# Optimization experiments

Hardware: AMD Instinct MI355X
Metric: run time of the kernel (lower is better)

The kernel has to match this reference:

```python
import jax, jax.numpy as jnp
import numpy as np

N_NODES = 50000
N_EDGES = 800000
IN_DIM = 128
HID = 64
ZDIM = 64
N_GRAPHS = 64


def gcn_conv(x, W, b, src, dst, n):
    # PyG GCNConv: add self-loops, symmetric deg^-1/2 normalization,
    # linear transform then gather-scatter aggregation.
    h = x @ W  # [N, out]
    loops = jnp.arange(n, dtype=src.dtype)
    s = jnp.concatenate([src, loops])
    d = jnp.concatenate([dst, loops])
    deg = jnp.zeros((n,), h.dtype).at[d].add(1.0)  # includes self-loops -> >=1
    dinv = jax.lax.rsqrt(deg)
    norm = dinv[s] * dinv[d]  # [E+N]
    msg = h[s] * norm[:, None]  # gather [E+N, out]
    out = jnp.zeros_like(h).at[d].add(msg)  # scatter-add
    return out + b


def mean_pool(h, batch, num_graphs):
    sums = jax.ops.segment_sum(h, batch, num_segments=num_graphs)
    cnt = jax.ops.segment_sum(jnp.ones((h.shape[0],), h.dtype), batch,
                              num_segments=num_graphs)
    return sums / jnp.maximum(cnt, 1.0)[:, None]


def setup_inputs() -> dict:
    key = jax.random.key(0)
    ks = jax.random.split(key, 9)
    x = jax.random.normal(ks[0], (N_NODES, IN_DIM), jnp.float32)
    edge_index = jax.random.randint(ks[1], (2, N_EDGES), 0, N_NODES, jnp.int64 if jax.config.jax_enable_x64 else jnp.int32)
    batch = jnp.sort(jax.random.randint(ks[2], (N_NODES,), 0, N_GRAPHS))
    s1 = 1.0 / np.sqrt(IN_DIM)
    s2 = 1.0 / np.sqrt(HID)
    W1 = jax.random.uniform(ks[3], (IN_DIM, HID), jnp.float32, -s1, s1)
    b1 = jnp.zeros((HID,), jnp.float32)
    Wmu = jax.random.uniform(ks[4], (HID, ZDIM), jnp.float32, -s2, s2)
    bmu = jnp.zeros((ZDIM,), jnp.float32)
    Wsig = jax.random.uniform(ks[5], (HID, ZDIM), jnp.float32, -s2, s2)
    bsig = jnp.zeros((ZDIM,), jnp.float32)
    return {"x": x, "edge_index": edge_index, "batch": batch,
            "num_graphs": N_GRAPHS, "W1": W1, "b1": b1,
            "Wmu": Wmu, "bmu": bmu, "Wsig": Wsig, "bsig": bsig}


def reference(x, edge_index, batch, num_graphs, W1, b1, Wmu, bmu, Wsig, bsig):
    src, dst = edge_index[0], edge_index[1]
    n = x.shape[0]
    h = jax.nn.elu(gcn_conv(x, W1, b1, src, dst, n))
    z_mu = mean_pool(jax.nn.elu(gcn_conv(h, Wmu, bmu, src, dst, n)), batch, num_graphs)
    z_sigma = mean_pool(jax.nn.elu(gcn_conv(h, Wsig, bsig, src, dst, n)), batch, num_graphs)
    return (z_mu, z_sigma)
```

## Files before the change

### kernel.cpp

```cpp
#include <hip/hip_runtime.h>
#include <hip/hip_fp16.h>


#define IN_DIM 128
#define HID 64
#define ZDIM 64
#define N_GRAPHS 64
#define SCAN_B 1024

typedef _Float16 half8 __attribute__((ext_vector_type(8)));
typedef float f32x4 __attribute__((ext_vector_type(4)));

__device__ __forceinline__ float elu1(float x) {
    return x > 0.f ? x : expm1f(x);
}

#define ACC8(RV, MV) do { \
    const __half2* _hp = (const __half2*)&(RV); \
    float2 _f0 = __half22float2(_hp[0]); \
    float2 _f1 = __half22float2(_hp[1]); \
    float2 _f2 = __half22float2(_hp[2]); \
    float2 _f3 = __half22float2(_hp[3]); \
    acc[0] = fmaf((MV), _f0.x, acc[0]); \
    acc[1] = fmaf((MV), _f0.y, acc[1]); \
    acc[2] = fmaf((MV), _f1.x, acc[2]); \
    acc[3] = fmaf((MV), _f1.y, acc[3]); \
    acc[4] = fmaf((MV), _f2.x, acc[4]); \
    acc[5] = fmaf((MV), _f2.y, acc[5]); \
    acc[6] = fmaf((MV), _f3.x, acc[6]); \
    acc[7] = fmaf((MV), _f3.y, acc[7]); \
  } while (0)

__global__ __launch_bounds__(256) void k_count_wfrag(const int* __restrict__ dst,
                                                     int* __restrict__ kc,
                                                     int* __restrict__ rank, int E,
                                                     const float* __restrict__ W1,
                                                     const float* __restrict__ Wmu,
                                                     const float* __restrict__ Wsig,
                                                     __half* __restrict__ F1,
                                                     __half* __restrict__ Fmu,
                                                     __half* __restrict__ Fsig,
                                                     int cntBlocks) {
    if ((int)blockIdx.x < cntBlocks) {
        int e = (blockIdx.x * 256 + threadIdx.x) * 2;
        if (e + 1 < E) {
            int2 d2 = *(const int2*)&dst[e];
            int r0 = atomicAdd(&kc[d2.x], 1);
            int r1 = atomicAdd(&kc[d2.y], 1);
            *(int2*)&rank[e] = make_int2(r0, r1);
        } else if (e < E) {
            rank[e] = atomicAdd(&kc[dst[e]], 1);
        }
        return;
    }
    int e = (blockIdx.x - cntBlocks) * 256 + threadIdx.x;
    if (e < 8192) {
        int j = e & 7, l = (e >> 3) & 63, ct = (e >> 9) & 3, ks = e >> 11;
        F1[e] = __float2half(W1[(ks * 32 + ((l >> 4) & 3) * 8 + j) * 64 + ct * 16 + (l & 15)]);
    }
    if (e < 4096) {
        int j = e & 7, l = (e >> 3) & 63, ct = (e >> 9) & 3, ks = e >> 11;
        int widx = (ks * 32 + ((l >> 4) & 3) * 8 + j) * 64 + ct * 16 + (l & 15);
        Fmu[e] = __float2half(Wmu[widx]);
        Fsig[e] = __float2half(Wsig[widx]);
    }
}

__global__ __launch_bounds__(SCAN_B) void k_scan1(const int* __restrict__ kc,
                                                  int* __restrict__ bsum, int n) {
    __shared__ int wpart[16];
    int tid = threadIdx.x, lane = tid & 63, w = tid >> 6;
    int i = blockIdx.x * SCAN_B + tid;
    int v = (i < n) ? kc[i] : 0;
#pragma unroll
    for (int d = 1; d < 64; d <<= 1) v += __shfl_xor(v, d, 64);
    if (lane == 0) wpart[w] = v;
    __syncthreads();
    if (tid < 16) {
        int t = wpart[tid];
#pragma unroll
        for (int d = 1; d < 16; d <<= 1) t += __shfl_xor(t, d, 64);
        if (tid == 0) bsum[blockIdx.x] = t;
    }
}

__global__ __launch_bounds__(SCAN_B) void k_scan3(const int* __restrict__ kc,
                                                  const int* __restrict__ bsum,
                                                  int* __restrict__ offs,
                                                  float* __restrict__ dinv,
                                                  int n, int nb) {
    __shared__ int wsum[16];
    __shared__ int sbase;
    int tid = threadIdx.x, lane = tid & 63, w = tid >> 6;
    if (tid < 64) {
        int v = (tid < nb) ? bsum[tid] : 0;
        int s = v;
#pragma unroll
        for (int d = 1; d < 64; d <<= 1) {
            int u = __shfl_up(s, d, 64);
            if (tid >= d) s += u;
        }
        if (tid == blockIdx.x) sbase = s - v;
    }
    int i = blockIdx.x * SCAN_B + tid;
    int v = (i < n) ? kc[i] : 0;
    int s = v;
#pragma unroll
    for (int d = 1; d < 64; d <<= 1) {
        int u = __shfl_up(s, d, 64);
        if (lane >= d) s += u;
    }
    if (lane == 63) wsum[w] = s;
    __syncthreads();
    if (tid < 16) {
        int t = wsum[tid];
#pragma unroll
        for (int d = 1; d < 16; d <<= 1) {
            int u = __shfl_up(t, d, 64);
            if (tid >= d) t += u;
        }
        wsum[tid] = t;
    }
    __syncthreads();
    int base = sbase + ((w == 0) ? 0 : wsum[w - 1]);
    if (i < n) {
        offs[i + 1] = base + s;
        dinv[i] = 1.0f / sqrtf(1.0f + (float)v);
        if (i == 0) offs[0] = 0;
    }
}

__global__ __launch_bounds__(256) void k_fill_mm1(const int* __restrict__ src,
                                                  const int* __restrict__ dst,
                                                  const int* __restrict__ rank,
                                                  const int* __restrict__ offs,
                                                  int* __restrict__ csr, int E,
                                                  const float* __restrict__ x,
                                                  const __half* __restrict__ F1,
                                                  const float* __restrict__ dinv,
                                                  __half* __restrict__ tsA,
                                                  __half* __restrict__ tsB, int n,
                                                  int fillBlocks) {
    if ((int)blockIdx.x < fillBlocks) {
        int e = (blockIdx.x * 256 + threadIdx.x) * 2;
        if (e + 1 < E) {
            int2 s2 = *(const int2*)&src[e];
            int2 d2 = *(const int2*)&dst[e];
            int2 r2 = *(const int2*)&rank[e];
            csr[offs[d2.x] + r2.x] = s2.x;
            csr[offs[d2.y] + r2.y] = s2.y;
        } else if (e < E) {
            csr[offs[dst[e]] + rank[e]] = src[e];
        }
        return;
    }
    int bid = blockIdx.x - fillBlocks;
    int l = threadIdx.x & 63;
    int wave = threadIdx.x >> 6;
    int m0 = bid * 64 + wave * 16;
    int row_a = m0 + (l & 15);
    if (row_a >= n) row_a = n - 1;
    int kg = l >> 4;

    f32x4 acc0 = {0.f, 0.f, 0.f, 0.f};
    f32x4 acc1 = acc0, acc2 = acc0, acc3 = acc0;

    const float* xr = x + (size_t)row_a * IN_DIM + kg * 8;
#pragma unroll
    for (int ks = 0; ks < 4; ++ks) {
        float4 xa = *(const float4*)(xr + ks * 32);
        float4 xb = *(const float4*)(xr + ks * 32 + 4);
        half8 a;
        a[0] = (_Float16)xa.x; a[1] = (_Float16)xa.y;
        a[2] = (_Float16)xa.z; a[3] = (_Float16)xa.w;
        a[4] = (_Float16)xb.x; a[5] = (_Float16)xb.y;
        a[6] = (_Float16)xb.z; a[7] = (_Float16)xb.w;
        const __half* fb = F1 + ((size_t)(ks * 4) * 64 + l) * 8;
        half8 b0 = *(const half8*)(fb);
        half8 b1 = *(const half8*)(fb + 512);
        half8 b2 = *(const half8*)(fb + 1024);
        half8 b3 = *(const half8*)(fb + 1536);
        acc0 = __builtin_amdgcn_mfma_f32_16x16x32_f16(a, b0, acc0, 0, 0, 0);
        acc1 = __builtin_amdgcn_mfma_f32_16x16x32_f16(a, b1, acc1, 0, 0, 0);
        acc2 = __builtin_amdgcn_mfma_f32_16x16x32_f16(a, b2, acc2, 0, 0, 0);
        acc3 = __builtin_amdgcn_mfma_f32_16x16x32_f16(a, b3, acc3, 0, 0, 0);
    }
    int col = l & 15;
#pragma unroll
    for (int r = 0; r < 4; ++r) {
        int row = m0 + kg * 4 + r;
        if (row < n) {
            float di = dinv[row];
            __half* pA = &tsA[(size_t)row * 32 + col];
            pA[0]  = __float2half(acc0[r] * di);
            pA[16] = __float2half(acc1[r] * di);
            __half* pB = &tsB[(size_t)row * 32 + col];
            pB[0]  = __float2half(acc2[r] * di);
            pB[16] = __float2half(acc3[r] * di);
        }
    }
}

__global__ __launch_bounds__(256) void k_gather_hh(const int* __restrict__ off,
                                                   const int* __restrict__ csr,
                                                   const float* __restrict__ dinv,
                                                   const __half* __restrict__ tsA,
                                                   const __half* __restrict__ tsB,
                                                   const float* __restrict__ b1,
                                                   __half* __restrict__ hhA,
                                                   __half* __restrict__ hhB, int n) {
    int bid = blockIdx.x;
    int half = (bid >> 2) & 1;
    int jb = (bid >> 3) * 4 + (bid & 3);
    int wv = threadIdx.x >> 6;
    int node0 = jb * 8 + wv * 2;
    if (node0 >= n) return;
    const __half* T = half ? tsB : tsA;
    __half* H = half ? hhB : hhA;
    int lane = threadIdx.x & 63;
    int nsel = lane >> 5;
    int node = node0 + nsel;
    bool valid = node < n;
    int nodec = valid ? node : n - 1;
    int l32 = lane & 31, g = l32 >> 2, sub = l32 & 3;
    int s0 = off[nodec], s1 = off[nodec + 1];
    float acc[8];
#pragma unroll
    for (int j = 0; j < 8; ++j) acc[j] = 0.f;

    if (s1 > s0) {
        int last = s1 - 1;
        int p0 = s0 + g, p1 = p0 + 8, p2 = p0 + 16, p3 = p0 + 24;
        int i0 = csr[p0 < s1 ? p0 : last];
        int i1 = csr[p1 < s1 ? p1 : last];
        int i2 = csr[p2 < s1 ? p2 : last];
        int i3 = csr[p3 < s1 ? p3 : last];
        float4 r0 = *(const float4*)&T[(size_t)i0 * 32 + sub * 8];
        float4 r1 = *(const float4*)&T[(size_t)i1 * 32 + sub * 8];
        float4 r2 = *(const float4*)&T[(size_t)i2 * 32 + sub * 8];
        float4 r3 = *(const float4*)&T[(size_t)i3 * 32 + sub * 8];
        float m0 = (p0 < s1) ? 1.f : 0.f;
        float m1 = (p1 < s1) ? 1.f : 0.f;
        float m2 = (p2 < s1) ? 1.f : 0.f;
        float m3 = (p3 < s1) ? 1.f : 0.f;
        ACC8(r0, m0);
        ACC8(r1, m1);
        ACC8(r2, m2);
        ACC8(r3, m3);
        for (int k = s0 + 32 + g; k < s1; k += 8) {
            int iv = csr[k];
            float4 rv = *(const float4*)&T[(size_t)iv * 32 + sub * 8];
            ACC8(rv, 1.f);
        }
    }

#pragma unroll
    for (int j = 0; j < 8; ++j) {
        acc[j] += __shfl_xor(acc[j], 4, 64);
        acc[j] += __shfl_xor(acc[j], 8, 64);
        acc[j] += __shfl_xor(acc[j], 16, 64);
    }

    if (g == 0 && valid) {
        int e0 = sub * 8;
        float4 sr = *(const float4*)&T[(size_t)nodec * 32 + e0];
        const __half2* sh = (const __half2*)&sr;
        float di = dinv[nodec];
        const float* bh = b1 + half * 32 + e0;
        float4 ba = *(const float4*)bh;
        float4 bb = *(const float4*)(bh + 4);
        float2 f0 = __half22float2(sh[0]);
        float2 f1 = __half22float2(sh[1]);
        float2 f2 = __half22float2(sh[2]);
        float2 f3 = __half22float2(sh[3]);
        float e0v = elu1((acc[0] + f0.x) * di + ba.x) * di;
        float e1v = elu1((acc[1] + f0.y) * di + ba.y) * di;
        float e2v = elu1((acc[2] + f1.x) * di + ba.z) * di;
        float e3v = elu1((acc[3] + f1.y) * di + ba.w) * di;
        float e4v = elu1((acc[4] + f2.x) * di + bb.x) * di;
        float e5v = elu1((acc[5] + f2.y) * di + bb.y) * di;
        float e6v = elu1((acc[6] + f3.x) * di + bb.z) * di;
        float e7v = elu1((acc[7] + f3.y) * di + bb.w) * di;
        float4 outv;
        __half2* op = (__half2*)&outv;
        op[0] = __floats2half2_rn(e0v, e1v);
        op[1] = __floats2half2_rn(e2v, e3v);
        op[2] = __floats2half2_rn(e4v, e5v);
        op[3] = __floats2half2_rn(e6v, e7v);
        *(float4*)&H[(size_t)node * 32 + e0] = outv;
    }
}

__global__ __launch_bounds__(256) void k_gather_g(const int* __restrict__ off,
                                                  const int* __restrict__ csr,
                                                  const float* __restrict__ dinv,
                                                  const __half* __restrict__ hhA,
                                                  const __half* __restrict__ hhB,
                                                  __half* __restrict__ gh2, int n) {
    int bid = blockIdx.x;
    int half = (bid >> 2) & 1;
    int jb = (bid >> 3) * 4 + (bid & 3);
    int wv = threadIdx.x >> 6;
    int node0 = jb * 8 + wv * 2;
    if (node0 >= n) return;
    const __half* T = half ? hhB : hhA;
    int lane = threadIdx.x & 63;
    int nsel = lane >> 5;
    int node = node0 + nsel;
    bool valid = node < n;
    int nodec = valid ? node : n - 1;
    int l32 = lane & 31, g = l32 >> 2, sub = l32 & 3;
    int s0 = off[nodec], s1 = off[nodec + 1];
    float acc[8];
#pragma unroll
    for (int j = 0; j < 8; ++j) acc[j] = 0.f;

    if (s1 > s0) {
        int last = s1 - 1;
        int p0 = s0 + g, p1 = p0 + 8, p2 = p0 + 16, p3 = p0 + 24;
        int i0 = csr[p0 < s1 ? p0 : last];
        int i1 = csr[p1 < s1 ? p1 : last];
        int i2 = csr[p2 < s1 ? p2 : last];
        int i3 = csr[p3 < s1 ? p3 : last];
        float4 r0 = *(const float4*)&T[(size_t)i0 * 32 + sub * 8];
        float4 r1 = *(const float4*)&T[(size_t)i1 * 32 + sub * 8];
        float4 r2 = *(const float4*)&T[(size_t)i2 * 32 + sub * 8];
        float4 r3 = *(const float4*)&T[(size_t)i3 * 32 + sub * 8];
        float m0 = (p0 < s1) ? 1.f : 0.f;
        float m1 = (p1 < s1) ? 1.f : 0.f;
        float m2 = (p2 < s1) ? 1.f : 0.f;
        float m3 = (p3 < s1) ? 1.f : 0.f;
        ACC8(r0, m0);
        ACC8(r1, m1);
        ACC8(r2, m2);
        ACC8(r3, m3);
        for (int k = s0 + 32 + g; k < s1; k += 8) {
            int iv = csr[k];
            float4 rv = *(const float4*)&T[(size_t)iv * 32 + sub * 8];
            ACC8(rv, 1.f);
        }
    }

#pragma unroll
    for (int j = 0; j < 8; ++j) {
        acc[j] += __shfl_xor(acc[j], 4, 64);
        acc[j] += __shfl_xor(acc[j], 8, 64);
        acc[j] += __shfl_xor(acc[j], 16, 64);
    }

    if (g == 0 && valid) {
        int e0 = sub * 8;
        float4 sr = *(const float4*)&T[(size_t)nodec * 32 + e0];
        const __half2* sh = (const __half2*)&sr;
        float di = dinv[nodec];
        float2 f0 = __half22float2(sh[0]);
        float2 f1 = __half22float2(sh[1]);
        float2 f2 = __half22float2(sh[2]);
        float2 f3 = __half22float2(sh[3]);
        float4 outv;
        __half2* op = (__half2*)&outv;
        op[0] = __floats2half2_rn((acc[0] + f0.x) * di, (acc[1] + f0.y) * di);
        op[1] = __floats2half2_rn((acc[2] + f1.x) * di, (acc[3] + f1.y) * di);
        op[2] = __floats2half2_rn((acc[4] + f2.x) * di, (acc[5] + f2.y) * di);
        op[3] = __floats2half2_rn((acc[6] + f3.x) * di, (acc[7] + f3.y) * di);
        *(float4*)&gh2[(size_t)node * 64 + half * 32 + e0] = outv;
    }
}

__global__ __launch_bounds__(256) void k_mm_pool(const __half* __restrict__ gh2,
                                                 const __half* __restrict__ Fmu,
                                                 const __half* __restrict__ Fsig,
                                                 const float* __restrict__ bmu,
                                                 const float* __restrict__ bsig,
                                                 const int* __restrict__ batch,
                                                 float* __restrict__ sums, int n) {
    __shared__ float wc[64 * 132];
    __shared__ int bs[64];
    const int tid = threadIdx.x;
    int l = tid & 63, wave = tid >> 6;
    int m0 = blockIdx.x * 64;
    int row_a = m0 + wave * 16 + (l & 15);
    if (row_a >= n) row_a = n - 1;
    int kg = l >> 4;

    f32x4 am[4], as[4];
#pragma unroll
    for (int ct = 0; ct < 4; ++ct) {
        am[ct] = (f32x4){0.f, 0.f, 0.f, 0.f};
        as[ct] = (f32x4){0.f, 0.f, 0.f, 0.f};
    }

    const __half* gr = gh2 + (size_t)row_a * 64 + kg * 8;
#pragma unroll
    for (int ks = 0; ks < 2; ++ks) {
        half8 a = *(const half8*)(gr + ks * 32);
        const __half* fm = Fmu + ((size_t)(ks * 4) * 64 + l) * 8;
        const __half* fs = Fsig + ((size_t)(ks * 4) * 64 + l) * 8;
#pragma unroll
        for (int ct = 0; ct < 4; ++ct) {
            half8 bm = *(const half8*)(fm + ct * 512);
            half8 bv = *(const half8*)(fs + ct * 512);
            am[ct] = __builtin_amdgcn_mfma_f32_16x16x32_f16(a, bm, am[ct], 0, 0, 0);
            as[ct] = __builtin_amdgcn_mfma_f32_16x16x32_f16(a, bv, as[ct], 0, 0, 0);
        }
    }

    if (tid < 64) bs[tid] = (m0 + tid < n) ? batch[m0 + tid] : -1;

    int col = l & 15;
#pragma unroll
    for (int ct = 0; ct < 4; ++ct) {
        float bM = bmu[ct * 16 + col];
        float bS = bsig[ct * 16 + col];
#pragma unroll
        for (int r = 0; r < 4; ++r) {
            int rr = wave * 16 + kg * 4 + r;
            wc[rr * 132 + ct * 16 + col] = elu1(am[ct][r] + bM);
            wc[rr * 132 + 64 + ct * 16 + col] = elu1(as[ct][r] + bS);
        }
    }
    __syncthreads();

    int d = tid & 127, seg = tid >> 7;
    int base = (d < 64) ? d : (64 * 64 - 64 + d);
    float acc = 0.f;
    int gcur = -1;
    int r0 = seg * 32;
    for (int r = r0; r < r0 + 32; ++r) {
        int gb = bs[r];
        if (gb < 0) break;
        float v = wc[r * 132 + d];
        if (gb != gcur) {
            if (gcur >= 0) atomicAdd(&sums[base + gcur * 64], acc);
            acc = 0.f;
            gcur = gb;
        }
        acc += v;
    }
    if (gcur >= 0) atomicAdd(&sums[base + gcur * 64], acc);
}

__global__ void k_pool_final(const float* __restrict__ sums,
                             const int* __restrict__ batch,
                             float* __restrict__ out, int n) {
    int i = blockIdx.x * blockDim.x + threadIdx.x;
    if (i >= 2 * N_GRAPHS * ZDIM) return;
    int g = (i >> 6) & 63;
    int lo = 0, hi = n;
    while (lo < hi) { int m = (lo + hi) >> 1; if (batch[m] < g) lo = m + 1; else hi = m; }
    int s = lo;
    lo = s; hi = n;
    while (lo < hi) { int m = (lo + hi) >> 1; if (batch[m] < g + 1) lo = m + 1; else hi = m; }
    float c = fmaxf((float)(lo - s), 1.0f);
    out[i] = sums[i] / c;
}

extern "C" void kernel_launch(void* const* d_in, const int* in_sizes, int n_in,
                              void* d_out, int out_size, void* d_ws, size_t ws_size,
                              hipStream_t stream) {
    const float* x    = (const float*)d_in[0];
    const int*   ei   = (const int*)d_in[1];
    const int*   batch= (const int*)d_in[2];
    const float* W1   = (const float*)d_in[4];
    const float* b1   = (const float*)d_in[5];
    const float* Wmu  = (const float*)d_in[6];
    const float* bmu  = (const float*)d_in[7];
    const float* Wsig = (const float*)d_in[8];
    const float* bsig = (const float*)d_in[9];
    float* out = (float*)d_out;

    const int n = in_sizes[0] / IN_DIM;
    const int E = in_sizes[1] / 2;
    const int* src = ei;
    const int* dst = ei + E;
    const int NSB = (n + SCAN_B - 1) / SCAN_B;

    float* ws = (float*)d_ws;
    size_t off_w = 0;
    int*   kc   = (int*)(ws + off_w); off_w += 50048;
    float* sums = ws + off_w; off_w += 8192;
    float* dinv = ws + off_w; off_w += 50048;
    int*   offs = (int*)(ws + off_w); off_w += 50056;
    int*   bsum = (int*)(ws + off_w); off_w += 64;
    int*   rank = (int*)(ws + off_w); off_w += 800000;
    int*   csr  = (int*)(ws + off_w); off_w += 800000;
    off_w = (off_w + 15) & ~(size_t)15;
    __half* F1   = (__half*)(ws + off_w); off_w += 4096;
    __half* Fmu  = (__half*)(ws + off_w); off_w += 2048;
    __half* Fsig = (__half*)(ws + off_w); off_w += 2048;
    const size_t HALFF = (size_t)50048 * 16;
    __half* tsA = (__half*)(ws + off_w); off_w += HALFF;
    __half* tsB = (__half*)(ws + off_w); off_w += HALFF;
    __half* hhA = (__half*)(ws + off_w); off_w += HALFF;
    __half* hhB = (__half*)(ws + off_w); off_w += HALFF;
    __half* gh2 = (__half*)(ws + off_w); off_w += (size_t)50048 * 32;

    const int gE2 = (E + 511) / 512;
    const int NB  = (n + 63) / 64;
    const int bph = (n + 7) / 8;
    const int bph4 = (bph + 3) & ~3;
    const int gG = 2 * bph4;

    hipMemsetAsync(kc, 0, (50048 + 8192) * sizeof(int), stream);
    k_count_wfrag<<<gE2 + 32, 256, 0, stream>>>(dst, kc, rank, E,
                                                W1, Wmu, Wsig, F1, Fmu, Fsig, gE2);
    k_scan1<<<NSB, SCAN_B, 0, stream>>>(kc, bsum, n);
    k_scan3<<<NSB, SCAN_B, 0, stream>>>(kc, bsum, offs, dinv, n, NSB);

    k_fill_mm1<<<gE2 + NB, 256, 0, stream>>>(src, dst, rank, offs, csr, E,
                                             x, F1, dinv, tsA, tsB, n, gE2);

    k_gather_hh<<<gG, 256, 0, stream>>>(offs, csr, dinv, tsA, tsB, b1, hhA, hhB, n);

    k_gather_g<<<gG, 256, 0, stream>>>(offs, csr, dinv, hhA, hhB, gh2, n);

    k_mm_pool<<<NB, 256, 0, stream>>>(gh2, Fmu, Fsig, bmu, bsig, batch, sums, n);
    k_pool_final<<<(2 * N_GRAPHS * ZDIM + 255) / 256, 256, 0, stream>>>(sums, batch, out, n);
}
```

Before: 214.1 us.

## Fuse second-layer gather into MFMA pooling kernel via shared-memory staging

Merges the second gather (aggregating hh over neighbours) into the matmul+pool kernel. Each block gathers its 64 nodes into LDS with full 64-wide rows, then runs the MFMA and pooling from LDS. The hh layout becomes one interleaved 64-wide buffer instead of two 32-wide halves. This removes a kernel launch and the gh2 write/read round trip through global memory. In exchange, each wave now walks 16 nodes one after another, which lowers parallelism and latency hiding during the gather and may lower occupancy because of the extra LDS.

```diff
diff --git a/kernel.cpp b/kernel.cpp
--- a/kernel.cpp
+++ b/kernel.cpp
@@ -207,8 +207,7 @@
                                                    const __half* __restrict__ tsA,
                                                    const __half* __restrict__ tsB,
                                                    const float* __restrict__ b1,
-                                                   __half* __restrict__ hhA,
-                                                   __half* __restrict__ hhB, int n) {
+                                                   __half* __restrict__ hh, int n) {
     int bid = blockIdx.x;
     int half = (bid >> 2) & 1;
     int jb = (bid >> 3) * 4 + (bid & 3);
@@ -216,7 +215,6 @@
     int node0 = jb * 8 + wv * 2;
     if (node0 >= n) return;
     const __half* T = half ? tsB : tsA;
-    __half* H = half ? hhB : hhA;
     int lane = threadIdx.x & 63;
     int nsel = lane >> 5;
     int node = node0 + nsel;
@@ -287,101 +285,95 @@
         op[1] = __floats2half2_rn(e2v, e3v);
         op[2] = __floats2half2_rn(e4v, e5v);
         op[3] = __floats2half2_rn(e6v, e7v);
-        *(float4*)&H[(size_t)node * 32 + e0] = outv;
-    }
-}
-
-__global__ __launch_bounds__(256) void k_gather_g(const int* __restrict__ off,
+        *(float4*)&hh[(size_t)node * 64 + half * 32 + e0] = outv;
+    }
+}
+
+__global__ __launch_bounds__(256) void k_mmg_pool(const int* __restrict__ off,
                                                   const int* __restrict__ csr,
                                                   const float* __restrict__ dinv,
-                                                  const __half* __restrict__ hhA,
-                                                  const __half* __restrict__ hhB,
-                                                  __half* __restrict__ gh2, int n) {
-    int bid = blockIdx.x;
-    int half = (bid >> 2) & 1;
-    int jb = (bid >> 3) * 4 + (bid & 3);
-    int wv = threadIdx.x >> 6;
-    int node0 = jb * 8 + wv * 2;
-    if (node0 >= n) return;
-    const __half* T = half ? hhB : hhA;
-    int lane = threadIdx.x & 63;
-    int nsel = lane >> 5;
-    int node = node0 + nsel;
-    bool valid = node < n;
-    int nodec = valid ? node : n - 1;
-    int l32 = lane & 31, g = l32 >> 2, sub = l32 & 3;
-    int s0 = off[nodec], s1 = off[nodec + 1];
-    float acc[8];
-#pragma unroll
-    for (int j = 0; j < 8; ++j) acc[j] = 0.f;
-
-    if (s1 > s0) {
-        int last = s1 - 1;
-        int p0 = s0 + g, p1 = p0 + 8, p2 = p0 + 16, p3 = p0 + 24;
-        int i0 = csr[p0 < s1 ? p0 : last];
-        int i1 = csr[p1 < s1 ? p1 : last];
-        int i2 = csr[p2 < s1 ? p2 : last];
-        int i3 = csr[p3 < s1 ? p3 : last];
-        float4 r0 = *(const float4*)&T[(size_t)i0 * 32 + sub * 8];
-        float4 r1 = *(const float4*)&T[(size_t)i1 * 32 + sub * 8];
-        float4 r2 = *(const float4*)&T[(size_t)i2 * 32 + sub * 8];
-        float4 r3 = *(const float4*)&T[(size_t)i3 * 32 + sub * 8];
-        float m0 = (p0 < s1) ? 1.f : 0.f;
-        float m1 = (p1 < s1) ? 1.f : 0.f;
-        float m2 = (p2 < s1) ? 1.f : 0.f;
-        float m3 = (p3 < s1) ? 1.f : 0.f;
-        ACC8(r0, m0);
-        ACC8(r1, m1);
-        ACC8(r2, m2);
-        ACC8(r3, m3);
-        for (int k = s0 + 32 + g; k < s1; k += 8) {
-            int iv = csr[k];
-            float4 rv = *(const float4*)&T[(size_t)iv * 32 + sub * 8];
-            ACC8(rv, 1.f);
-        }
-    }
-
-#pragma unroll
-    for (int j = 0; j < 8; ++j) {
-        acc[j] += __shfl_xor(acc[j], 4, 64);
-        acc[j] += __shfl_xor(acc[j], 8, 64);
-        acc[j] += __shfl_xor(acc[j], 16, 64);
-    }
-
-    if (g == 0 && valid) {
-        int e0 = sub * 8;
-        float4 sr = *(const float4*)&T[(size_t)nodec * 32 + e0];
-        const __half2* sh = (const __half2*)&sr;
-        float di = dinv[nodec];
-        float2 f0 = __half22float2(sh[0]);
-        float2 f1 = __half22float2(sh[1]);
-        float2 f2 = __half22float2(sh[2]);
-        float2 f3 = __half22float2(sh[3]);
-        float4 outv;
-        __half2* op = (__half2*)&outv;
-        op[0] = __floats2half2_rn((acc[0] + f0.x) * di, (acc[1] + f0.y) * di);
-        op[1] = __floats2half2_rn((acc[2] + f1.x) * di, (acc[3] + f1.y) * di);
-        op[2] = __floats2half2_rn((acc[4] + f2.x) * di, (acc[5] + f2.y) * di);
-        op[3] = __floats2half2_rn((acc[6] + f3.x) * di, (acc[7] + f3.y) * di);
-        *(float4*)&gh2[(size_t)node * 64 + half * 32 + e0] = outv;
-    }
-}
-
-__global__ __launch_bounds__(256) void k_mm_pool(const __half* __restrict__ gh2,
-                                                 const __half* __restrict__ Fmu,
-                                                 const __half* __restrict__ Fsig,
-                                                 const float* __restrict__ bmu,
-                                                 const float* __restrict__ bsig,
-                                                 const int* __restrict__ batch,
-                                                 float* __restrict__ sums, int n) {
+                                                  const __half* __restrict__ hh,
+                                                  const __half* __restrict__ Fmu,
+                                                  const __half* __restrict__ Fsig,
+                                                  const float* __restrict__ bmu,
+                                                  const float* __restrict__ bsig,
+                                                  const int* __restrict__ batch,
+                                                  float* __restrict__ sums, int n) {
     __shared__ float wc[64 * 132];
+    __shared__ __half gs[64 * 72];
     __shared__ int bs[64];
     const int tid = threadIdx.x;
-    int l = tid & 63, wave = tid >> 6;
+    int lane = tid & 63, wave = tid >> 6;
     int m0 = blockIdx.x * 64;
-    int row_a = m0 + wave * 16 + (l & 15);
-    if (row_a >= n) row_a = n - 1;
-    int kg = l >> 4;
+    int g = lane >> 3, sub = lane & 7;
+
+    for (int t = 0; t < 16; ++t) {
+        int node = m0 + wave * 16 + t;
+        bool valid = node < n;
+        int nodec = valid ? node : n - 1;
+        int s0 = off[nodec], s1 = off[nodec + 1];
+        float acc[8];
+#pragma unroll
+        for (int j = 0; j < 8; ++j) acc[j] = 0.f;
+
+        if (s1 > s0) {
+            int last = s1 - 1;
+            int p0 = s0 + g, p1 = p0 + 8, p2 = p0 + 16, p3 = p0 + 24;
+            int i0 = csr[p0 < s1 ? p0 : last];
+            int i1 = csr[p1 < s1 ? p1 : last];
+            int i2 = csr[p2 < s1 ? p2 : last];
+            int i3 = csr[p3 < s1 ? p3 : last];
+            float4 r0 = *(const float4*)&hh[(size_t)i0 * 64 + sub * 8];
+            float4 r1 = *(const float4*)&hh[(size_t)i1 * 64 + sub * 8];
+            float4 r2 = *(const float4*)&hh[(size_t)i2 * 64 + sub * 8];
+            float4 r3 = *(const float4*)&hh[(size_t)i3 * 64 + sub * 8];
+            float m0v = (p0 < s1) ? 1.f : 0.f;
+            float m1v = (p1 < s1) ? 1.f : 0.f;
+            float m2v = (p2 < s1) ? 1.f : 0.f;
+            float m3v = (p3 < s1) ? 1.f : 0.f;
+            ACC8(r0, m0v);
+            ACC8(r1, m1v);
+            ACC8(r2, m2v);
+            ACC8(r3, m3v);
+            for (int k = s0 + 32 + g; k < s1; k += 8) {
+                int iv = csr[k];
+                float4 rv = *(const float4*)&hh[(size_t)iv * 64 + sub * 8];
+                ACC8(rv, 1.f);
+            }
+        }
+
+#pragma unroll
+        for (int j = 0; j < 8; ++j) {
+            acc[j] += __shfl_xor(acc[j], 8, 64);
+            acc[j] += __shfl_xor(acc[j], 16, 64);
+            acc[j] += __shfl_xor(acc[j], 32, 64);
+        }
+
+        if (g == 0) {
+            int row = wave * 16 + t;
+            float4 outv = make_float4(0.f, 0.f, 0.f, 0.f);
+            if (valid) {
+                float4 sr = *(const float4*)&hh[(size_t)nodec * 64 + sub * 8];
+                const __half2* sh = (const __half2*)&sr;
+                float di = dinv[nodec];
+                float2 f0 = __half22float2(sh[0]);
+                float2 f1 = __half22float2(sh[1]);
+                float2 f2 = __half22float2(sh[2]);
+                float2 f3 = __half22float2(sh[3]);
+                __half2* op = (__half2*)&outv;
+                op[0] = __floats2half2_rn((acc[0] + f0.x) * di, (acc[1] + f0.y) * di);
+                op[1] = __floats2half2_rn((acc[2] + f1.x) * di, (acc[3] + f1.y) * di);
+                op[2] = __floats2half2_rn((acc[4] + f2.x) * di, (acc[5] + f2.y) * di);
+                op[3] = __floats2half2_rn((acc[6] + f3.x) * di, (acc[7] + f3.y) * di);
+            }
+            *(float4*)&gs[row * 72 + sub * 8] = outv;
+        }
+    }
+    if (tid < 64) bs[tid] = (m0 + tid < n) ? batch[m0 + tid] : -1;
+    __syncthreads();
+
+    int row_l = wave * 16 + (lane & 15);
+    int kg = lane >> 4;
 
     f32x4 am[4], as[4];
 #pragma unroll
@@ -390,12 +382,11 @@
         as[ct] = (f32x4){0.f, 0.f, 0.f, 0.f};
     }
 
-    const __half* gr = gh2 + (size_t)row_a * 64 + kg * 8;
 #pragma unroll
     for (int ks = 0; ks < 2; ++ks) {
-        half8 a = *(const half8*)(gr + ks * 32);
-        const __half* fm = Fmu + ((size_t)(ks * 4) * 64 + l) * 8;
-        const __half* fs = Fsig + ((size_t)(ks * 4) * 64 + l) * 8;
+        half8 a = *(const half8*)&gs[row_l * 72 + kg * 8 + ks * 32];
+        const __half* fm = Fmu + ((size_t)(ks * 4) * 64 + lane) * 8;
+        const __half* fs = Fsig + ((size_t)(ks * 4) * 64 + lane) * 8;
 #pragma unroll
         for (int ct = 0; ct < 4; ++ct) {
             half8 bm = *(const half8*)(fm + ct * 512);
@@ -405,9 +396,7 @@
         }
     }
 
-    if (tid < 64) bs[tid] = (m0 + tid < n) ? batch[m0 + tid] : -1;
-
-    int col = l & 15;
+    int col = lane & 15;
 #pragma unroll
     for (int ct = 0; ct < 4; ++ct) {
         float bM = bmu[ct * 16 + col];
@@ -491,9 +480,7 @@
     const size_t HALFF = (size_t)50048 * 16;
     __half* tsA = (__half*)(ws + off_w); off_w += HALFF;
     __half* tsB = (__half*)(ws + off_w); off_w += HALFF;
-    __half* hhA = (__half*)(ws + off_w); off_w += HALFF;
-    __half* hhB = (__half*)(ws + off_w); off_w += HALFF;
-    __half* gh2 = (__half*)(ws + off_w); off_w += (size_t)50048 * 32;
+    __half* hh  = (__half*)(ws + off_w); off_w += (size_t)50048 * 32;
 
     const int gE2 = (E + 511) / 512;
     const int NB  = (n + 63) / 64;
@@ -510,10 +497,9 @@
     k_fill_mm1<<<gE2 + NB, 256, 0, stream>>>(src, dst, rank, offs, csr, E,
                                              x, F1, dinv, tsA, tsB, n, gE2);
 
-    k_gather_hh<<<gG, 256, 0, stream>>>(offs, csr, dinv, tsA, tsB, b1, hhA, hhB, n);
-
-    k_gather_g<<<gG, 256, 0, stream>>>(offs, csr, dinv, hhA, hhB, gh2, n);
-
-    k_mm_pool<<<NB, 256, 0, stream>>>(gh2, Fmu, Fsig, bmu, bsig, batch, sums, n);
+    k_gather_hh<<<gG, 256, 0, stream>>>(offs, csr, dinv, tsA, tsB, b1, hh, n);
+
+    k_mmg_pool<<<NB, 256, 0, stream>>>(offs, csr, dinv, hh, Fmu, Fsig,
+                                       bmu, bsig, batch, sums, n);
     k_pool_final<<<(2 * N_GRAPHS * ZDIM + 255) / 256, 256, 0, stream>>>(sums, batch, out, n);
 }
```

New measurement: 248.0 us. 15.8% more time.
